# Performance work log

Measured on AMD Instinct MI355X. Metric: run time of the kernel, lower is better.

The kernel has to match this reference:

```python
import jax, jax.numpy as jnp
import numpy as np

N, L, E = 2, 2048, 1024
H = 16
HD = E // H
FF = 4 * E
EPS = 1e-5


def _layer_norm(x, g, b):
    mu = jnp.mean(x, axis=-1, keepdims=True)
    var = jnp.mean((x - mu) ** 2, axis=-1, keepdims=True)
    return (x - mu) * jax.lax.rsqrt(var + EPS) * g + b


def setup_inputs() -> dict:
    key = jax.random.key(0)
    ks = jax.random.split(key, 9)
    s = 0.02
    return {
        "value": jax.random.normal(ks[0], (N, L, E), jnp.float32),
        "key": jax.random.normal(ks[1], (N, L, E), jnp.float32),
        "query": jax.random.normal(ks[2], (N, L, E), jnp.float32),
        "w_out": jax.random.normal(ks[3], (E, E), jnp.float32) * s,
        "b_out": jnp.zeros((E,), jnp.float32),
        "w1": jax.random.normal(ks[4], (E, FF), jnp.float32) * s,
        "b1": jnp.zeros((FF,), jnp.float32),
        "w2": jax.random.normal(ks[5], (FF, E), jnp.float32) * s,
        "b2": jnp.zeros((E,), jnp.float32),
        "g1": jnp.ones((E,), jnp.float32),
        "be1": jnp.zeros((E,), jnp.float32),
        "g2": jnp.ones((E,), jnp.float32),
        "be2": jnp.zeros((E,), jnp.float32),
    }


def reference(value, key, query, w_out, b_out, w1, b1, w2, b2, g1, be1, g2, be2):
    # NOTE: source module never applies its Q/K/V Linear layers (repo bug);
    # raw inputs are reshaped per-head and used directly.
    v = value.reshape(N, L, H, HD)
    k = key.reshape(N, L, H, HD)
    q = query.reshape(N, L, H, HD)
    # energy: [N, H, Lq, Lk]; scale is 1/sqrt(embed_size) per the source
    energy = jnp.einsum("nqhd,nkhd->nhqk", q, k)
    attn = jax.nn.softmax(energy / jnp.sqrt(jnp.float32(E)), axis=-1)
    out = jnp.einsum("nhql,nlhd->nqhd", attn, v).reshape(N, L, E)
    out = out @ w_out + b_out
    x = _layer_norm(out + query, g1, be1)
    ff = jax.nn.relu(x @ w1 + b1) @ w2 + b2
    return _layer_norm(ff + x, g2, be2)
```

## Files before the change

kernel.cpp:

```cpp
#include <hip/hip_runtime.h>
#include <hip/hip_bf16.h>

#define NB 2
#define LL 2048
#define EE 1024
#define HH 16
#define HDD 64
#define FFD 4096

typedef unsigned short ushort_t;
typedef __attribute__((ext_vector_type(8))) short short8;
typedef __attribute__((ext_vector_type(4))) float f32x4;

constexpr float LN_EPS = 1e-5f;
constexpr float QSCALE = 0.03125f * 1.44269504088896340736f;

__device__ inline ushort_t f2bf(float f) {
    union { __hip_bfloat16 b; ushort_t u; } v;
    v.b = __float2bfloat16(f);
    return v.u;
}
__device__ inline float bf2f(unsigned us) {
    union { unsigned u; float f; } v; v.u = us << 16; return v.f;
}
__device__ inline unsigned pk_hi16(float lo, float hi) {
    const unsigned sel = 0x07060302u;
    unsigned r;
    asm("v_perm_b32 %0, %1, %2, %3" : "=v"(r) : "v"(hi), "v"(lo), "s"(sel));
    return r;
}

__device__ inline void gload16(const void* g, void* lds) {
    __builtin_amdgcn_global_load_lds(
        (const __attribute__((address_space(1))) void*)g,
        (__attribute__((address_space(3))) void*)lds, 16, 0, 0);
}

__global__ __launch_bounds__(256) void k_cvt(
    const float* __restrict__ in, ushort_t* __restrict__ out)
{
    const int t = threadIdx.x;
    const int g = blockIdx.x * 32 + (t >> 3);
    const int n = g >> 15, h = (g >> 11) & 15, l2 = g & 2047;
    const int d0 = (t & 7) * 8;
    const float* src = in + ((size_t)(n * LL + l2) * HH + h) * HDD + d0;
    const float4 a = *(const float4*)src;
    const float4 b = *(const float4*)(src + 4);
    uint4 pk;
    pk.x = f2bf(a.x) | ((unsigned)f2bf(a.y) << 16);
    pk.y = f2bf(a.z) | ((unsigned)f2bf(a.w) << 16);
    pk.z = f2bf(b.x) | ((unsigned)f2bf(b.y) << 16);
    pk.w = f2bf(b.z) | ((unsigned)f2bf(b.w) << 16);
    *(uint4*)(out + (size_t)g * HDD + d0) = pk;
}

__global__ __launch_bounds__(256) void v_cvt_t(
    const float* __restrict__ in, ushort_t* __restrict__ out)
{
    __shared__ float T[64][68];
    const int lb = blockIdx.x, h = blockIdx.y, n = blockIdx.z;
    const int t = threadIdx.x;
    const int l0 = lb * 64;
    {
        const int r = t >> 2, c0 = (t & 3) * 16;
        const float* src = in + ((size_t)(n * LL + l0 + r) * HH + h) * HDD + c0;
#pragma unroll
        for (int i = 0; i < 4; ++i)
            *(float4*)&T[r][c0 + 4 * i] = *(const float4*)(src + 4 * i);
    }
    __syncthreads();
    {
        const int d = t >> 2, tq = t & 3;
        unsigned u[8];
#pragma unroll
        for (int k = 0; k < 8; ++k) {
            const int c0 = tq * 16 + 2 * k, c1 = c0 + 1;
            const int p0 = (((c0 >> 5) * 2 + ((c0 >> 2) & 1)) << 4) +
                           (((c0 >> 3) & 3) << 2) + (c0 & 3);
            const int p1 = (((c1 >> 5) * 2 + ((c1 >> 2) & 1)) << 4) +
                           (((c1 >> 3) & 3) << 2) + (c1 & 3);
            u[k] = f2bf(T[p0][d]) | ((unsigned)f2bf(T[p1][d]) << 16);
        }
        ushort_t* dst = out + ((size_t)(n * HH + h) * HDD + d) * LL + l0 + tq * 16;
        uint4 q0; q0.x = u[0]; q0.y = u[1]; q0.z = u[2]; q0.w = u[3];
        uint4 q1; q1.x = u[4]; q1.y = u[5]; q1.z = u[6]; q1.w = u[7];
        *(uint4*)(dst)     = q0;
        *(uint4*)(dst + 8) = q1;
    }
}

__global__ __launch_bounds__(256) void attn_mfma(
    const float* __restrict__ Qf,
    const ushort_t* __restrict__ Kh,
    const ushort_t* __restrict__ Vt,
    ushort_t* __restrict__ O)
{
    const int s = blockIdx.x;
    const int xcd = s & 7, seq = s >> 3;
    const int qb = seq & 31, tt = seq >> 5;
    const int h = ((tt & 1) << 3) | xcd;
    const int n = tt >> 1;

    const int t = threadIdx.x, w = t >> 6, l = t & 63;
    const int lr = l & 15, lg = l >> 4;

    __shared__ __align__(16) ushort_t Kl[3][64 * 64];
    __shared__ __align__(16) ushort_t Vl[2][64 * 64];

    const size_t hbase = ((size_t)n * HH + h) * LL * HDD;
    const size_t vbase = ((size_t)n * HH + h) * HDD * LL;
    const int q0 = qb * 64 + w * 16;

    short8 bq[2];
#pragma unroll
    for (int ks = 0; ks < 2; ++ks) {
        const float* qsrc = Qf + ((size_t)(n * LL + q0 + lr) * HH + h) * HDD
                               + ks * 32 + lg * 8;
        const float4 a = *(const float4*)qsrc;
        const float4 b = *(const float4*)(qsrc + 4);
        union { short8 s8; unsigned u[4]; } pk;
        pk.u[0] = f2bf(a.x * QSCALE) | ((unsigned)f2bf(a.y * QSCALE) << 16);
        pk.u[1] = f2bf(a.z * QSCALE) | ((unsigned)f2bf(a.w * QSCALE) << 16);
        pk.u[2] = f2bf(b.x * QSCALE) | ((unsigned)f2bf(b.y * QSCALE) << 16);
        pk.u[3] = f2bf(b.z * QSCALE) | ((unsigned)f2bf(b.w * QSCALE) << 16);
        bq[ks] = pk.s8;
    }

    union { short8 s8; ushort_t u[8]; } one_u;
#pragma unroll
    for (int i = 0; i < 8; ++i) one_u.u[i] = 0x3F80;
    const short8 ones = one_u.s8;

    f32x4 acco[4];
#pragma unroll
    for (int dn = 0; dn < 4; ++dn) {
        f32x4 z = {0.f, 0.f, 0.f, 0.f};
        acco[dn] = z;
    }
    f32x4 accp = {0.f, 0.f, 0.f, 0.f};

    const int id0 = w * 2;
#define STAGEK(buf, kt)                                                        \
    {                                                                          \
        _Pragma("unroll")                                                      \
        for (int j = 0; j < 2; ++j) {                                          \
            const int id = (id0 + j) * 64 + l;                                 \
            const int r = id >> 3, c = id & 7;                                 \
            const int cs = c ^ (r & 7);                                        \
            gload16(Kh + hbase + (size_t)((kt) * 64 + r) * HDD + cs * 8,       \
                    (void*)(Kl[buf] + (id0 + j) * 512));                       \
        }                                                                      \
    }
#define STAGEV(buf, kt)                                                        \
    {                                                                          \
        _Pragma("unroll")                                                      \
        for (int j = 0; j < 2; ++j) {                                          \
            const int id = (id0 + j) * 64 + l;                                 \
            const int r = id >> 3, c = id & 7;                                 \
            const int cs = c ^ (r & 7);                                        \
            gload16(Vt + vbase + (size_t)r * LL + (kt) * 64 + cs * 8,          \
                    (void*)(Vl[buf] + (id0 + j) * 512));                       \
        }                                                                      \
    }

    constexpr int NT = LL / 64;
    const f32x4 z4 = {0.f, 0.f, 0.f, 0.f};

    STAGEK(0, 0);
    STAGEK(1, 1);
    STAGEV(0, 0);
    STAGEK(2, 2);
    STAGEV(1, 1);
    asm volatile("s_waitcnt vmcnt(4)" ::: "memory");
    __builtin_amdgcn_sched_barrier(0);
    __builtin_amdgcn_s_barrier();

    f32x4 accsA[4], accsB[4];
    {
        short8 ak[4];
#pragma unroll
        for (int nk = 0; nk < 4; ++nk) {
            const int row = nk * 16 + lr;
            ak[nk] = *(const short8*)(Kl[0] + row * 64 + ((lg) ^ (row & 7)) * 8);
        }
#pragma unroll
        for (int nk = 0; nk < 4; ++nk)
            accsA[nk] = __builtin_amdgcn_mfma_f32_16x16x32_bf16(
                ak[nk], bq[0], z4, 0, 0, 0);
#pragma unroll
        for (int nk = 0; nk < 4; ++nk) {
            const int row = nk * 16 + lr;
            ak[nk] = *(const short8*)(Kl[0] + row * 64 + ((4 | lg) ^ (row & 7)) * 8);
        }
#pragma unroll
        for (int nk = 0; nk < 4; ++nk)
            accsA[nk] = __builtin_amdgcn_mfma_f32_16x16x32_bf16(
                ak[nk], bq[1], accsA[nk], 0, 0, 0);
    }

    int ks3 = 0, kn = 1;

#define ATTN_BODY(O_, N_, VB_, KT_)                                            \
    {                                                                          \
        const ushort_t* kb_ = Kl[kn];                                          \
        __builtin_amdgcn_s_setprio(1);                                         \
        {                                                                      \
            short8 ak[4];                                                      \
            _Pragma("unroll")                                                  \
            for (int nk = 0; nk < 4; ++nk) {                                   \
                const int row = nk * 16 + lr;                                  \
                ak[nk] = *(const short8*)(kb_ + row * 64 + ((lg) ^ (row & 7)) * 8); \
            }                                                                  \
            _Pragma("unroll")                                                  \
            for (int nk = 0; nk < 4; ++nk)                                     \
                N_[nk] = __builtin_amdgcn_mfma_f32_16x16x32_bf16(              \
                    ak[nk], bq[0], z4, 0, 0, 0);                               \
            _Pragma("unroll")                                                  \
            for (int nk = 0; nk < 4; ++nk) {                                   \
                const int row = nk * 16 + lr;                                  \
                ak[nk] = *(const short8*)(kb_ + row * 64 + ((4 | lg) ^ (row & 7)) * 8); \
            }                                                                  \
            _Pragma("unroll")                                                  \
            for (int nk = 0; nk < 4; ++nk)                                     \
                N_[nk] = __builtin_amdgcn_mfma_f32_16x16x32_bf16(              \
                    ak[nk], bq[1], N_[nk], 0, 0, 0);                           \
        }                                                                      \
        __builtin_amdgcn_s_setprio(0);                                         \
        float p[4][4];                                                         \
        _Pragma("unroll")                                                      \
        for (int nk = 0; nk < 4; ++nk) {                                       \
            _Pragma("unroll")                                                  \
            for (int r = 0; r < 4; ++r)                                        \
                p[nk][r] = __builtin_amdgcn_exp2f(O_[nk][r]);                  \
        }                                                                      \
        short8 pa[2];                                                          \
        _Pragma("unroll")                                                      \
        for (int ks2 = 0; ks2 < 2; ++ks2) {                                    \
            union { short8 s8; unsigned u[4]; } pk;                            \
            pk.u[0] = pk_hi16(p[2 * ks2][0], p[2 * ks2][1]);                   \
            pk.u[1] = pk_hi16(p[2 * ks2][2], p[2 * ks2][3]);                   \
            pk.u[2] = pk_hi16(p[2 * ks2 + 1][0], p[2 * ks2 + 1][1]);           \
            pk.u[3] = pk_hi16(p[2 * ks2 + 1][2], p[2 * ks2 + 1][3]);           \
            pa[ks2] = pk.s8;                                                   \
        }                                                                      \
        __builtin_amdgcn_s_setprio(1);                                         \
        _Pragma("unroll")                                                      \
        for (int ks2 = 0; ks2 < 2; ++ks2) {                                    \
            short8 bv[4];                                                      \
            _Pragma("unroll")                                                  \
            for (int dn = 0; dn < 4; ++dn) {                                   \
                const int row = dn * 16 + lr;                                  \
                bv[dn] = *(const short8*)(                                     \
                    Vl[VB_] + row * 64 + (((ks2 << 2) | lg) ^ (row & 7)) * 8); \
            }                                                                  \
            accp = __builtin_amdgcn_mfma_f32_16x16x32_bf16(pa[ks2], ones,      \
                                                           accp, 0, 0, 0);    \
            _Pragma("unroll")                                                  \
            for (int dn = 0; dn < 4; ++dn)                                     \
                acco[dn] = __builtin_amdgcn_mfma_f32_16x16x32_bf16(            \
                    pa[ks2], bv[dn], acco[dn], 0, 0, 0);                       \
        }                                                                      \
        __builtin_amdgcn_s_setprio(0);                                         \
        __builtin_amdgcn_s_barrier();                                          \
        STAGEK(ks3, (KT_) + 3);                                                \
        STAGEV(VB_, (KT_) + 2);                                                \
        asm volatile("s_waitcnt vmcnt(4)" ::: "memory");                       \
        __builtin_amdgcn_sched_barrier(0);                                     \
        __builtin_amdgcn_s_barrier();                                          \
        { const int tnk = kn + 1; ks3 = kn; kn = (tnk == 3) ? 0 : tnk; }       \
    }

    for (int kt = 0; kt < NT; kt += 2) {
        ATTN_BODY(accsA, accsB, 0, kt);
        ATTN_BODY(accsB, accsA, 1, kt + 1);
    }

#pragma unroll
    for (int r = 0; r < 4; ++r) {
        const float invl = 1.f / accp[r];
        const int qq = q0 + lg * 4 + r;
        ushort_t* dst = O + (size_t)(n * LL + qq) * EE + h * HDD + lr;
#pragma unroll
        for (int dn = 0; dn < 4; ++dn)
            dst[dn * 16] = f2bf(acco[dn][r] * invl);
    }
#undef ATTN_BODY
#undef STAGEK
#undef STAGEV
}

__global__ __launch_bounds__(256) void tcvt(
    const float* __restrict__ in, ushort_t* __restrict__ out, int K, int N)
{
    __shared__ float T[32][36];
    const int n0 = blockIdx.x * 32, k0 = blockIdx.y * 32;
    const int r = threadIdx.x >> 3, c4 = (threadIdx.x & 7) * 4;
    const float4 v = *(const float4*)(in + (size_t)(k0 + r) * N + n0 + c4);
    T[r][c4] = v.x; T[r][c4 + 1] = v.y; T[r][c4 + 2] = v.z; T[r][c4 + 3] = v.w;
    __syncthreads();
    const unsigned a = f2bf(T[c4][r])     | ((unsigned)f2bf(T[c4 + 1][r]) << 16);
    const unsigned b = f2bf(T[c4 + 2][r]) | ((unsigned)f2bf(T[c4 + 3][r]) << 16);
    uint2 pk; pk.x = a; pk.y = b;
    *(uint2*)(out + (size_t)(n0 + r) * K + k0 + c4) = pk;
}

__global__ __launch_bounds__(512, 2) void gemm8p(
    const ushort_t* __restrict__ A, const ushort_t* __restrict__ Bt,
    const float* __restrict__ bias, ushort_t* __restrict__ C,
    int M, int N, int K)
{
    __shared__ __align__(16) ushort_t L[2][4][256 * 32];

    const int tid = threadIdx.x;
    const int w = tid >> 6, l = tid & 63;
    const int fr = l & 15, lg = l >> 4;
    const int wr = w >> 2, wc = w & 3;

    const int gx = gridDim.x;
    const int nwg = gx * gridDim.y;
    const int bid = blockIdx.y * gx + blockIdx.x;
    int tile = bid;
    if ((nwg & 7) == 0) tile = (bid & 7) * (nwg >> 3) + (bid >> 3);
    const int bx = tile % gx, by = tile / gx;
    const int brow = by * 256, bcol = bx * 256;

    const int NT = K >> 6;
    const int UMAX = NT << 2;

#define STAGE8(u)                                                              \
    if ((u) < UMAX) {                                                          \
        const int tt = (u) >> 2, slot = (u) & 3;                               \
        const int op = slot & 1, kh = slot >> 1;                               \
        const ushort_t* sp = op ? Bt : A;                                      \
        const int rb = op ? bcol : brow;                                       \
        ushort_t* db = (ushort_t*)L[tt & 1][slot];                             \
        _Pragma("unroll")                                                      \
        for (int j = 0; j < 2; ++j) {                                          \
            const int id = j * 512 + tid;                                      \
            const int row = id >> 2, c = id & 3;                               \
            const int cs = c ^ ((row >> 1) & 3);                               \
            gload16(sp + (size_t)(rb + row) * K + tt * 64 + kh * 32 + cs * 8,  \
                    (void*)(db + id * 8));                                     \
        }                                                                      \
    }

    f32x4 acc[8][4];
#pragma unroll
    for (int i = 0; i < 8; ++i)
#pragma unroll
        for (int g = 0; g < 4; ++g) { f32x4 zz = {0.f,0.f,0.f,0.f}; acc[i][g] = zz; }

#pragma unroll
    for (int u = 0; u < 6; ++u) STAGE8(u);
    asm volatile("s_waitcnt vmcnt(4)" ::: "memory");
    __builtin_amdgcn_sched_barrier(0);
    __builtin_amdgcn_s_barrier();

    const int iters = NT >> 1;
    for (int it = 0; it < iters; ++it) {
#pragma unroll
        for (int p = 0; p < 8; ++p) {
            STAGE8(it * 8 + p + 6);
            const int d  = p >> 2;
            const int mh = p & 1, kh = (p >> 1) & 1;
            short8 af[4], bfr[4];
#pragma unroll
            for (int f = 0; f < 4; ++f) {
                const int row = wr * 128 + (mh * 4 + f) * 16 + fr;
                const int ch = lg ^ ((row >> 1) & 3);
                af[f] = *(const short8*)(&L[d][kh * 2][row * 32 + ch * 8]);
            }
#pragma unroll
            for (int g = 0; g < 4; ++g) {
                const int row = wc * 64 + g * 16 + fr;
                const int ch = lg ^ ((row >> 1) & 3);
                bfr[g] = *(const short8*)(&L[d][kh * 2 + 1][row * 32 + ch * 8]);
            }
            __builtin_amdgcn_s_barrier();
            __builtin_amdgcn_s_setprio(1);
#pragma unroll
            for (int f = 0; f < 4; ++f)
#pragma unroll
                for (int g = 0; g < 4; ++g)
                    acc[mh * 4 + f][g] = __builtin_amdgcn_mfma_f32_16x16x32_bf16(
                        af[f], bfr[g], acc[mh * 4 + f][g], 0, 0, 0);
            __builtin_amdgcn_s_setprio(0);
            if (p == 3 || p == 7) {
                asm volatile("s_waitcnt vmcnt(4)" ::: "memory");
                __builtin_amdgcn_sched_barrier(0);
            }
            __builtin_amdgcn_s_barrier();
        }
    }

#pragma unroll
    for (int mi = 0; mi < 8; ++mi) {
#pragma unroll
        for (int g = 0; g < 4; ++g) {
            const int col = bcol + wc * 64 + g * 16 + fr;
            const float bv = bias[col];
#pragma unroll
            for (int r = 0; r < 4; ++r) {
                const int row = brow + wr * 128 + mi * 16 + lg * 4 + r;
                const float v = fmaxf(acc[mi][g][r] + bv, 0.f);
                C[(size_t)row * N + col] = f2bf(v);
            }
        }
    }
#undef STAGE8
}

#define SOFF(slot) ((slot) == 0 ? 0 : (slot) == 1 ? 8192 : (slot) == 2 ? 12288 : 20480)

template <int KSPLIT>
__global__ __launch_bounds__(512, 2) void gemm8p_n128(
    const ushort_t* __restrict__ A, const ushort_t* __restrict__ Bt,
    ushort_t* __restrict__ C, int M, int N, int K)
{
    __shared__ __align__(16) ushort_t L[2][24576];

    const int tid = threadIdx.x;
    const int w = tid >> 6, l = tid & 63;
    const int fr = l & 15, lg = l >> 4;
    const int wr = w >> 2, wc = w & 3;

    const int z = blockIdx.z;
    const int Keff = K / KSPLIT;
    const int kb = z * Keff;

    const int gx = gridDim.x;
    const int nwg = gx * gridDim.y;
    const int bid = blockIdx.y * gx + blockIdx.x;
    int tile = bid;
    if ((nwg & 7) == 0) tile = (bid & 7) * (nwg >> 3) + (bid >> 3);
    const int bx = tile % gx, by = tile / gx;
    const int brow = by * 256, bcol = bx * 128;

    const int NT = Keff >> 6;
    const int UMAX = NT << 2;

#define STG(u)                                                                 \
    if ((u) < UMAX) {                                                          \
        const int tt = (u) >> 2, slot = (u) & 3;                               \
        const int op = slot & 1, kh = slot >> 1;                               \
        const ushort_t* sp = op ? Bt : A;                                      \
        const int rb = op ? bcol : brow;                                       \
        ushort_t* db = (ushort_t*)L[tt & 1] + SOFF(slot);                      \
        const int nld = op ? 1 : 2;                                            \
        _Pragma("unroll")                                                      \
        for (int j = 0; j < nld; ++j) {                                        \
            const int id = j * 512 + tid;                                      \
            const int row = id >> 2, c = id & 3;                               \
            const int cs = c ^ ((row >> 1) & 3);                               \
            gload16(sp + (size_t)(rb + row) * K + kb + tt * 64 + kh * 32 + cs * 8, \
                    (void*)(db + id * 8));                                     \
        }                                                                      \
    }

    f32x4 acc[8][2];
#pragma unroll
    for (int i = 0; i < 8; ++i)
#pragma unroll
        for (int g = 0; g < 2; ++g) { f32x4 zz = {0.f,0.f,0.f,0.f}; acc[i][g] = zz; }

#pragma unroll
    for (int u = 0; u < 6; ++u) STG(u);
    asm volatile("s_waitcnt vmcnt(3)" ::: "memory");
    __builtin_amdgcn_sched_barrier(0);
    __builtin_amdgcn_s_barrier();

    const int iters = NT >> 1;
    for (int it = 0; it < iters; ++it) {
#pragma unroll
        for (int p = 0; p < 8; ++p) {
            STG(it * 8 + p + 6);
            const int d  = p >> 2;
            const int mh = p & 1, kh = (p >> 1) & 1;
            short8 af[4], bfr[2];
#pragma unroll
            for (int f = 0; f < 4; ++f) {
                const int row = wr * 128 + (mh * 4 + f) * 16 + fr;
                const int ch = lg ^ ((row >> 1) & 3);
                af[f] = *(const short8*)(&L[d][SOFF(kh * 2) + row * 32 + ch * 8]);
            }
#pragma unroll
            for (int g = 0; g < 2; ++g) {
                const int row = wc * 32 + g * 16 + fr;
                const int ch = lg ^ ((row >> 1) & 3);
                bfr[g] = *(const short8*)(&L[d][SOFF(kh * 2 + 1) + row * 32 + ch * 8]);
            }
            __builtin_amdgcn_s_barrier();
            __builtin_amdgcn_s_setprio(1);
#pragma unroll
            for (int f = 0; f < 4; ++f)
#pragma unroll
                for (int g = 0; g < 2; ++g)
                    acc[mh * 4 + f][g] = __builtin_amdgcn_mfma_f32_16x16x32_bf16(
                        af[f], bfr[g], acc[mh * 4 + f][g], 0, 0, 0);
            __builtin_amdgcn_s_setprio(0);
            if (p == 3 || p == 7) {
                asm volatile("s_waitcnt vmcnt(3)" ::: "memory");
                __builtin_amdgcn_sched_barrier(0);
            }
            __builtin_amdgcn_s_barrier();
        }
    }

    ushort_t* Cb = C + (size_t)z * M * N;
#pragma unroll
    for (int mi = 0; mi < 8; ++mi) {
#pragma unroll
        for (int g = 0; g < 2; ++g) {
            const int col = bcol + wc * 32 + g * 16 + fr;
#pragma unroll
            for (int r = 0; r < 4; ++r) {
                const int row = brow + wr * 128 + mi * 16 + lg * 4 + r;
                Cb[(size_t)row * N + col] = f2bf(acc[mi][g][r]);
            }
        }
    }
#undef STG
}

__global__ __launch_bounds__(256) void ln_mid(
    const ushort_t* __restrict__ y0, const ushort_t* __restrict__ y1,
    const float* __restrict__ qres, const float* __restrict__ b0,
    const float* __restrict__ g, const float* __restrict__ b,
    ushort_t* __restrict__ out)
{
    const int row = blockIdx.x;
    const int t = threadIdx.x;
    const size_t off = (size_t)row * EE;
    const uint2 a = ((const uint2*)(y0 + off))[t];
    const uint2 c = ((const uint2*)(y1 + off))[t];
    const float4 qq = ((const float4*)(qres + off))[t];
    const float4 b04 = ((const float4*)b0)[t];
    float x[4];
    x[0] = bf2f(a.x & 0xffff) + bf2f(c.x & 0xffff) + qq.x + b04.x;
    x[1] = bf2f(a.x >> 16)    + bf2f(c.x >> 16)    + qq.y + b04.y;
    x[2] = bf2f(a.y & 0xffff) + bf2f(c.y & 0xffff) + qq.z + b04.z;
    x[3] = bf2f(a.y >> 16)    + bf2f(c.y >> 16)    + qq.w + b04.w;

    float s = 0.f, ss = 0.f;
#pragma unroll
    for (int i = 0; i < 4; ++i) { s += x[i]; ss += x[i] * x[i]; }
#pragma unroll
    for (int o = 1; o < 64; o <<= 1) {
        s  += __shfl_xor(s, o, 64);
        ss += __shfl_xor(ss, o, 64);
    }
    __shared__ float sm[8];
    const int wid = t >> 6;
    if ((t & 63) == 0) { sm[wid * 2] = s; sm[wid * 2 + 1] = ss; }
    __syncthreads();
    const float stot  = sm[0] + sm[2] + sm[4] + sm[6];
    const float sstot = sm[1] + sm[3] + sm[5] + sm[7];
    const float mu  = stot * (1.f / EE);
    const float inv = rsqrtf(sstot * (1.f / EE) - mu * mu + LN_EPS);

    const float4 gg = ((const float4*)g)[t];
    const float4 bb = ((const float4*)b)[t];
    uint2 pk;
    pk.x = f2bf((x[0] - mu) * inv * gg.x + bb.x) |
           ((unsigned)f2bf((x[1] - mu) * inv * gg.y + bb.y) << 16);
    pk.y = f2bf((x[2] - mu) * inv * gg.z + bb.z) |
           ((unsigned)f2bf((x[3] - mu) * inv * gg.w + bb.w) << 16);
    ((uint2*)(out + off))[t] = pk;
}

__global__ __launch_bounds__(256) void ln_out(
    const ushort_t* __restrict__ y0, const ushort_t* __restrict__ y1,
    const ushort_t* __restrict__ xb, const float* __restrict__ b2,
    const float* __restrict__ g, const float* __restrict__ be,
    float* __restrict__ out)
{
    const int row = blockIdx.x;
    const int t = threadIdx.x;
    const size_t off = (size_t)row * EE;
    const uint2 a = ((const uint2*)(y0 + off))[t];
    const uint2 b = ((const uint2*)(y1 + off))[t];
    const uint2 c = ((const uint2*)(xb + off))[t];
    const float4 bb2 = ((const float4*)b2)[t];
    float x[4];
    x[0] = bf2f(a.x & 0xffff) + bf2f(b.x & 0xffff) + bf2f(c.x & 0xffff) + bb2.x;
    x[1] = bf2f(a.x >> 16)    + bf2f(b.x >> 16)    + bf2f(c.x >> 16)    + bb2.y;
    x[2] = bf2f(a.y & 0xffff) + bf2f(b.y & 0xffff) + bf2f(c.y & 0xffff) + bb2.z;
    x[3] = bf2f(a.y >> 16)    + bf2f(b.y >> 16)    + bf2f(c.y >> 16)    + bb2.w;

    float s = 0.f, ss = 0.f;
#pragma unroll
    for (int i = 0; i < 4; ++i) { s += x[i]; ss += x[i] * x[i]; }
#pragma unroll
    for (int o = 1; o < 64; o <<= 1) {
        s  += __shfl_xor(s, o, 64);
        ss += __shfl_xor(ss, o, 64);
    }
    __shared__ float sm[8];
    const int wid = t >> 6;
    if ((t & 63) == 0) { sm[wid * 2] = s; sm[wid * 2 + 1] = ss; }
    __syncthreads();
    const float stot  = sm[0] + sm[2] + sm[4] + sm[6];
    const float sstot = sm[1] + sm[3] + sm[5] + sm[7];
    const float mu  = stot * (1.f / EE);
    const float inv = rsqrtf(sstot * (1.f / EE) - mu * mu + LN_EPS);

    const float4 gg = ((const float4*)g)[t];
    const float4 bb = ((const float4*)be)[t];
    float4 o;
    o.x = (x[0] - mu) * inv * gg.x + bb.x;
    o.y = (x[1] - mu) * inv * gg.y + bb.y;
    o.z = (x[2] - mu) * inv * gg.z + bb.z;
    o.w = (x[3] - mu) * inv * gg.w + bb.w;
    ((float4*)(out + off))[t] = o;
}

extern "C" void kernel_launch(void* const* d_in, const int* in_sizes, int n_in,
                              void* d_out, int out_size, void* d_ws, size_t ws_size,
                              hipStream_t stream) {
    (void)in_sizes; (void)n_in; (void)out_size; (void)ws_size;
    const float* value = (const float*)d_in[0];
    const float* key   = (const float*)d_in[1];
    const float* query = (const float*)d_in[2];
    const float* w_out = (const float*)d_in[3];
    const float* b_out = (const float*)d_in[4];
    const float* w1    = (const float*)d_in[5];
    const float* b1    = (const float*)d_in[6];
    const float* w2    = (const float*)d_in[7];
    const float* b2    = (const float*)d_in[8];
    const float* g1    = (const float*)d_in[9];
    const float* be1   = (const float*)d_in[10];
    const float* g2    = (const float*)d_in[11];
    const float* be2   = (const float*)d_in[12];
    float* out = (float*)d_out;

    const int M = NB * LL;
    char* base = (char*)d_ws;
    ushort_t* attn_bf = (ushort_t*)(base);
    ushort_t* x_bf    = (ushort_t*)(base + (8ull  << 20));
    char*     hregion = base + (16ull << 20);
    ushort_t* h_bf    = (ushort_t*)hregion;
    ushort_t* Kh      = (ushort_t*)(hregion);
    ushort_t* Vt      = (ushort_t*)(hregion + (8ull  << 20));
    ushort_t* y01     = (ushort_t*)(base + (48ull << 20));
    ushort_t* w0T     = (ushort_t*)(base + (64ull << 20));
    ushort_t* w1T     = (ushort_t*)(base + (66ull << 20));
    ushort_t* w2T     = (ushort_t*)(base + (74ull << 20));

    tcvt<<<dim3(EE / 32, EE / 32), 256, 0, stream>>>(w_out, w0T, EE, EE);
    tcvt<<<dim3(FFD / 32, EE / 32), 256, 0, stream>>>(w1, w1T, EE, FFD);
    tcvt<<<dim3(EE / 32, FFD / 32), 256, 0, stream>>>(w2, w2T, FFD, EE);

    k_cvt<<<NB * HH * LL / 32, 256, 0, stream>>>(key, Kh);
    v_cvt_t<<<dim3(LL / 64, HH, NB), 256, 0, stream>>>(value, Vt);

    attn_mfma<<<dim3(NB * HH * LL / 64), 256, 0, stream>>>(query, Kh, Vt,
                                                           attn_bf);

    gemm8p_n128<2><<<dim3(EE / 128, M / 256, 2), 512, 0, stream>>>(
        attn_bf, w0T, y01, M, EE, EE);
    ln_mid<<<M, 256, 0, stream>>>(y01, y01 + (size_t)M * EE, query, b_out,
                                  g1, be1, x_bf);

    gemm8p<<<dim3(FFD / 256, M / 256), 512, 0, stream>>>(x_bf, w1T, b1, h_bf,
                                                         M, FFD, EE);
    gemm8p_n128<2><<<dim3(EE / 128, M / 256, 2), 512, 0, stream>>>(
        h_bf, w2T, y01, M, EE, FFD);
    ln_out<<<M, 256, 0, stream>>>(y01, y01 + (size_t)M * EE, x_bf, b2, g2, be2,
                                  out);
}
```

Before: 187.1 us.

## Merge preprocessing kernels into one launch and restage K prefetch earlier in attention

Folds the three weight-transpose launches and the K and V conversion launches into a single prep kernel that dispatches on block index, cutting four launches and their tails. In the attention kernel, the staging macros become precomputed per-thread pointers that advance by a stride each iteration. The next K tile load now issues at the start of each body instead of after the barrier, and an extra barrier is added after the prologue. This is meant to overlap K loads with the score MFMAs and cut address arithmetic, at the cost of another barrier and a larger shared-memory footprint for the weight blocks in prep.

```diff
diff --git a/kernel.cpp b/kernel.cpp
--- a/kernel.cpp
+++ b/kernel.cpp
@@ -36,56 +36,85 @@
         (__attribute__((address_space(3))) void*)lds, 16, 0, 0);
 }
 
-__global__ __launch_bounds__(256) void k_cvt(
-    const float* __restrict__ in, ushort_t* __restrict__ out)
+__global__ __launch_bounds__(256) void prep(
+    const float* __restrict__ w_out, const float* __restrict__ w1,
+    const float* __restrict__ w2, const float* __restrict__ key,
+    const float* __restrict__ value,
+    ushort_t* __restrict__ w0T, ushort_t* __restrict__ w1T,
+    ushort_t* __restrict__ w2T, ushort_t* __restrict__ Kh,
+    ushort_t* __restrict__ Vt)
 {
+    __shared__ float Tsh[64 * 68];
+    const int b = blockIdx.x;
     const int t = threadIdx.x;
-    const int g = blockIdx.x * 32 + (t >> 3);
-    const int n = g >> 15, h = (g >> 11) & 15, l2 = g & 2047;
-    const int d0 = (t & 7) * 8;
-    const float* src = in + ((size_t)(n * LL + l2) * HH + h) * HDD + d0;
-    const float4 a = *(const float4*)src;
-    const float4 b = *(const float4*)(src + 4);
-    uint4 pk;
-    pk.x = f2bf(a.x) | ((unsigned)f2bf(a.y) << 16);
-    pk.y = f2bf(a.z) | ((unsigned)f2bf(a.w) << 16);
-    pk.z = f2bf(b.x) | ((unsigned)f2bf(b.y) << 16);
-    pk.w = f2bf(b.z) | ((unsigned)f2bf(b.w) << 16);
-    *(uint4*)(out + (size_t)g * HDD + d0) = pk;
-}
-
-__global__ __launch_bounds__(256) void v_cvt_t(
-    const float* __restrict__ in, ushort_t* __restrict__ out)
-{
-    __shared__ float T[64][68];
-    const int lb = blockIdx.x, h = blockIdx.y, n = blockIdx.z;
-    const int t = threadIdx.x;
-    const int l0 = lb * 64;
-    {
-        const int r = t >> 2, c0 = (t & 3) * 16;
-        const float* src = in + ((size_t)(n * LL + l0 + r) * HH + h) * HDD + c0;
-#pragma unroll
-        for (int i = 0; i < 4; ++i)
-            *(float4*)&T[r][c0 + 4 * i] = *(const float4*)(src + 4 * i);
-    }
-    __syncthreads();
-    {
-        const int d = t >> 2, tq = t & 3;
-        unsigned u[8];
-#pragma unroll
-        for (int k = 0; k < 8; ++k) {
-            const int c0 = tq * 16 + 2 * k, c1 = c0 + 1;
-            const int p0 = (((c0 >> 5) * 2 + ((c0 >> 2) & 1)) << 4) +
-                           (((c0 >> 3) & 3) << 2) + (c0 & 3);
-            const int p1 = (((c1 >> 5) * 2 + ((c1 >> 2) & 1)) << 4) +
-                           (((c1 >> 3) & 3) << 2) + (c1 & 3);
-            u[k] = f2bf(T[p0][d]) | ((unsigned)f2bf(T[p1][d]) << 16);
-        }
-        ushort_t* dst = out + ((size_t)(n * HH + h) * HDD + d) * LL + l0 + tq * 16;
-        uint4 q0; q0.x = u[0]; q0.y = u[1]; q0.z = u[2]; q0.w = u[3];
-        uint4 q1; q1.x = u[4]; q1.y = u[5]; q1.z = u[6]; q1.w = u[7];
-        *(uint4*)(dst)     = q0;
-        *(uint4*)(dst + 8) = q1;
+
+    if (b < 9216) {
+        const float* in; ushort_t* outp; int K, N, bx, by;
+        if (b < 1024)      { in = w_out; outp = w0T; K = EE;  N = EE;
+                             bx = b & 31;             by = b >> 5; }
+        else if (b < 5120) { const int i = b - 1024; in = w1; outp = w1T;
+                             K = EE;  N = FFD; bx = i & 127; by = i >> 7; }
+        else               { const int i = b - 5120; in = w2; outp = w2T;
+                             K = FFD; N = EE;  bx = i & 31;  by = i >> 5; }
+        const int n0 = bx * 32, k0 = by * 32;
+        const int r = t >> 3, c4 = (t & 7) * 4;
+        const float4 v = *(const float4*)(in + (size_t)(k0 + r) * N + n0 + c4);
+        Tsh[r * 36 + c4]     = v.x; Tsh[r * 36 + c4 + 1] = v.y;
+        Tsh[r * 36 + c4 + 2] = v.z; Tsh[r * 36 + c4 + 3] = v.w;
+        __syncthreads();
+        const unsigned a = f2bf(Tsh[c4 * 36 + r]) |
+                           ((unsigned)f2bf(Tsh[(c4 + 1) * 36 + r]) << 16);
+        const unsigned bb = f2bf(Tsh[(c4 + 2) * 36 + r]) |
+                            ((unsigned)f2bf(Tsh[(c4 + 3) * 36 + r]) << 16);
+        uint2 pk; pk.x = a; pk.y = bb;
+        *(uint2*)(outp + (size_t)(n0 + r) * K + k0 + c4) = pk;
+    } else if (b < 11264) {
+        const int g = (b - 9216) * 32 + (t >> 3);
+        const int n = g >> 15, h = (g >> 11) & 15, l2 = g & 2047;
+        const int d0 = (t & 7) * 8;
+        const float* src = key + ((size_t)(n * LL + l2) * HH + h) * HDD + d0;
+        const float4 a = *(const float4*)src;
+        const float4 bb = *(const float4*)(src + 4);
+        uint4 pk;
+        pk.x = f2bf(a.x)  | ((unsigned)f2bf(a.y)  << 16);
+        pk.y = f2bf(a.z)  | ((unsigned)f2bf(a.w)  << 16);
+        pk.z = f2bf(bb.x) | ((unsigned)f2bf(bb.y) << 16);
+        pk.w = f2bf(bb.z) | ((unsigned)f2bf(bb.w) << 16);
+        *(uint4*)(Kh + (size_t)g * HDD + d0) = pk;
+    } else {
+        const int i = b - 11264;
+        const int lb = i & 31, h = (i >> 5) & 15, n = i >> 9;
+        const int l0 = lb * 64;
+        {
+            const int r = t >> 2, c0 = (t & 3) * 16;
+            const float* src = value +
+                ((size_t)(n * LL + l0 + r) * HH + h) * HDD + c0;
+#pragma unroll
+            for (int ii = 0; ii < 4; ++ii)
+                *(float4*)&Tsh[r * 68 + c0 + 4 * ii] =
+                    *(const float4*)(src + 4 * ii);
+        }
+        __syncthreads();
+        {
+            const int d = t >> 2, tq = t & 3;
+            unsigned u[8];
+#pragma unroll
+            for (int k = 0; k < 8; ++k) {
+                const int c0 = tq * 16 + 2 * k, c1 = c0 + 1;
+                const int p0 = (((c0 >> 5) * 2 + ((c0 >> 2) & 1)) << 4) +
+                               (((c0 >> 3) & 3) << 2) + (c0 & 3);
+                const int p1 = (((c1 >> 5) * 2 + ((c1 >> 2) & 1)) << 4) +
+                               (((c1 >> 3) & 3) << 2) + (c1 & 3);
+                u[k] = f2bf(Tsh[p0 * 68 + d]) |
+                       ((unsigned)f2bf(Tsh[p1 * 68 + d]) << 16);
+            }
+            ushort_t* dst = Vt + ((size_t)(n * HH + h) * HDD + d) * LL
+                               + l0 + tq * 16;
+            uint4 q0; q0.x = u[0]; q0.y = u[1]; q0.z = u[2]; q0.w = u[3];
+            uint4 q1; q1.x = u[4]; q1.y = u[5]; q1.z = u[6]; q1.w = u[7];
+            *(uint4*)(dst)     = q0;
+            *(uint4*)(dst + 8) = q1;
+        }
     }
 }
 
@@ -140,41 +169,34 @@
     f32x4 accp = {0.f, 0.f, 0.f, 0.f};
 
     const int id0 = w * 2;
-#define STAGEK(buf, kt)                                                        \
-    {                                                                          \
-        _Pragma("unroll")                                                      \
-        for (int j = 0; j < 2; ++j) {                                          \
-            const int id = (id0 + j) * 64 + l;                                 \
-            const int r = id >> 3, c = id & 7;                                 \
-            const int cs = c ^ (r & 7);                                        \
-            gload16(Kh + hbase + (size_t)((kt) * 64 + r) * HDD + cs * 8,       \
-                    (void*)(Kl[buf] + (id0 + j) * 512));                       \
-        }                                                                      \
-    }
-#define STAGEV(buf, kt)                                                        \
-    {                                                                          \
-        _Pragma("unroll")                                                      \
-        for (int j = 0; j < 2; ++j) {                                          \
-            const int id = (id0 + j) * 64 + l;                                 \
-            const int r = id >> 3, c = id & 7;                                 \
-            const int cs = c ^ (r & 7);                                        \
-            gload16(Vt + vbase + (size_t)r * LL + (kt) * 64 + cs * 8,          \
-                    (void*)(Vl[buf] + (id0 + j) * 512));                       \
-        }                                                                      \
-    }
+    const int idA = id0 * 64 + l,          idB = (id0 + 1) * 64 + l;
+    const int rA = idA >> 3,               rB = idB >> 3;
+    const int csA = (idA & 7) ^ (rA & 7),  csB = (idB & 7) ^ (rB & 7);
+    const ushort_t* kg = Kh + hbase;
+    const ushort_t* vg = Vt + vbase;
 
     constexpr int NT = LL / 64;
     const f32x4 z4 = {0.f, 0.f, 0.f, 0.f};
 
-    STAGEK(0, 0);
-    STAGEK(1, 1);
-    STAGEV(0, 0);
-    STAGEK(2, 2);
-    STAGEV(1, 1);
+    gload16(kg + (size_t)(rA) * HDD + csA * 8,        (void*)(Kl[0] + id0 * 512));
+    gload16(kg + (size_t)(rB) * HDD + csB * 8,        (void*)(Kl[0] + id0 * 512 + 512));
+    gload16(kg + (size_t)(64 + rA) * HDD + csA * 8,   (void*)(Kl[1] + id0 * 512));
+    gload16(kg + (size_t)(64 + rB) * HDD + csB * 8,   (void*)(Kl[1] + id0 * 512 + 512));
+    gload16(vg + (size_t)rA * LL + csA * 8,           (void*)(Vl[0] + id0 * 512));
+    gload16(vg + (size_t)rB * LL + csB * 8,           (void*)(Vl[0] + id0 * 512 + 512));
+    gload16(kg + (size_t)(128 + rA) * HDD + csA * 8,  (void*)(Kl[2] + id0 * 512));
+    gload16(kg + (size_t)(128 + rB) * HDD + csB * 8,  (void*)(Kl[2] + id0 * 512 + 512));
+    gload16(vg + (size_t)rA * LL + 64 + csA * 8,      (void*)(Vl[1] + id0 * 512));
+    gload16(vg + (size_t)rB * LL + 64 + csB * 8,      (void*)(Vl[1] + id0 * 512 + 512));
     asm volatile("s_waitcnt vmcnt(4)" ::: "memory");
     __builtin_amdgcn_sched_barrier(0);
     __builtin_amdgcn_s_barrier();
 
+    const ushort_t* kp0 = kg + (size_t)(192 + rA) * HDD + csA * 8;
+    const ushort_t* kp1 = kg + (size_t)(192 + rB) * HDD + csB * 8;
+    const ushort_t* vp0 = vg + (size_t)rA * LL + 128 + csA * 8;
+    const ushort_t* vp1 = vg + (size_t)rB * LL + 128 + csB * 8;
+
     f32x4 accsA[4], accsB[4];
     {
         short8 ak[4];
@@ -197,11 +219,16 @@
             accsA[nk] = __builtin_amdgcn_mfma_f32_16x16x32_bf16(
                 ak[nk], bq[1], accsA[nk], 0, 0, 0);
     }
+    __builtin_amdgcn_s_barrier();
 
     int ks3 = 0, kn = 1;
 
-#define ATTN_BODY(O_, N_, VB_, KT_)                                            \
+#define ATTN_BODY(O_, N_, VB_)                                                 \
     {                                                                          \
+              \
+        gload16(kp0, (void*)(Kl[ks3] + id0 * 512));                            \
+        gload16(kp1, (void*)(Kl[ks3] + id0 * 512 + 512));                      \
+        kp0 += 4096; kp1 += 4096;                                              \
         const ushort_t* kb_ = Kl[kn];                                          \
         __builtin_amdgcn_s_setprio(1);                                         \
         {                                                                      \
@@ -262,8 +289,9 @@
         }                                                                      \
         __builtin_amdgcn_s_setprio(0);                                         \
         __builtin_amdgcn_s_barrier();                                          \
-        STAGEK(ks3, (KT_) + 3);                                                \
-        STAGEV(VB_, (KT_) + 2);                                                \
+        gload16(vp0, (void*)(Vl[VB_] + id0 * 512));                            \
+        gload16(vp1, (void*)(Vl[VB_] + id0 * 512 + 512));                      \
+        vp0 += 64; vp1 += 64;                                                  \
         asm volatile("s_waitcnt vmcnt(4)" ::: "memory");                       \
         __builtin_amdgcn_sched_barrier(0);                                     \
         __builtin_amdgcn_s_barrier();                                          \
@@ -271,8 +299,8 @@
     }
 
     for (int kt = 0; kt < NT; kt += 2) {
-        ATTN_BODY(accsA, accsB, 0, kt);
-        ATTN_BODY(accsB, accsA, 1, kt + 1);
+        ATTN_BODY(accsA, accsB, 0);
+        ATTN_BODY(accsB, accsA, 1);
     }
 
 #pragma unroll
@@ -285,23 +313,6 @@
             dst[dn * 16] = f2bf(acco[dn][r] * invl);
     }
 #undef ATTN_BODY
-#undef STAGEK
-#undef STAGEV
-}
-
-__global__ __launch_bounds__(256) void tcvt(
-    const float* __restrict__ in, ushort_t* __restrict__ out, int K, int N)
-{
-    __shared__ float T[32][36];
-    const int n0 = blockIdx.x * 32, k0 = blockIdx.y * 32;
-    const int r = threadIdx.x >> 3, c4 = (threadIdx.x & 7) * 4;
-    const float4 v = *(const float4*)(in + (size_t)(k0 + r) * N + n0 + c4);
-    T[r][c4] = v.x; T[r][c4 + 1] = v.y; T[r][c4 + 2] = v.z; T[r][c4 + 3] = v.w;
-    __syncthreads();
-    const unsigned a = f2bf(T[c4][r])     | ((unsigned)f2bf(T[c4 + 1][r]) << 16);
-    const unsigned b = f2bf(T[c4 + 2][r]) | ((unsigned)f2bf(T[c4 + 3][r]) << 16);
-    uint2 pk; pk.x = a; pk.y = b;
-    *(uint2*)(out + (size_t)(n0 + r) * K + k0 + c4) = pk;
 }
 
 __global__ __launch_bounds__(512, 2) void gemm8p(
@@ -646,12 +657,8 @@
     ushort_t* w1T     = (ushort_t*)(base + (66ull << 20));
     ushort_t* w2T     = (ushort_t*)(base + (74ull << 20));
 
-    tcvt<<<dim3(EE / 32, EE / 32), 256, 0, stream>>>(w_out, w0T, EE, EE);
-    tcvt<<<dim3(FFD / 32, EE / 32), 256, 0, stream>>>(w1, w1T, EE, FFD);
-    tcvt<<<dim3(EE / 32, FFD / 32), 256, 0, stream>>>(w2, w2T, FFD, EE);
-
-    k_cvt<<<NB * HH * LL / 32, 256, 0, stream>>>(key, Kh);
-    v_cvt_t<<<dim3(LL / 64, HH, NB), 256, 0, stream>>>(value, Vt);
+    prep<<<12288, 256, 0, stream>>>(w_out, w1, w2, key, value,
+                                    w0T, w1T, w2T, Kh, Vt);
 
     attn_mfma<<<dim3(NB * HH * LL / 64), 256, 0, stream>>>(query, Kh, Vt,
                                                            attn_bf);
```

After: 178.2 us. 4.7% less time.
